# Performance work log

Hardware: AMD Instinct MI355X
Metric: run time of the kernel (lower is better)

The kernel has to match this reference:

```python
import jax, jax.numpy as jnp
import numpy as np
from jax import lax

B, C, H, W = 4096, 10, 30, 30
NCOL = C - 1                      # non-background colors 1..9
_pi, _pj = np.triu_indices(NCOL, 1)  # lexicographic (i<j) pair order, matches the python double loop
PI = jnp.asarray(_pi); PJ = jnp.asarray(_pj)
NPAIR = int(_pi.shape[0])         # 36
W_TRANSFORM, W_EXACT, W_AFFINE, W_ROT, W_REFL, W_GEO, W_EDGE, W_CBAL = 0.2, 7.0, 0.4, 0.3, 0.3, 0.5, 0.3, 0.2
GAMMA = 1.4


def setup_inputs() -> dict:
    key = jax.random.key(0)
    ks = jax.random.split(key, 6)
    pred = jax.random.normal(ks[0], (B, C, H, W), jnp.float32)
    tidx = jax.random.randint(ks[1], (B, H, W), 0, C)
    target = jnp.transpose(jax.nn.one_hot(tidx, C, dtype=jnp.float32), (0, 3, 1, 2))
    iidx = jax.random.randint(ks[2], (B, H, W), 0, C)
    input_grid = jnp.transpose(jax.nn.one_hot(iidx, C, dtype=jnp.float32), (0, 3, 1, 2))
    theta = 0.1 * jax.random.normal(ks[3], (B, 2, 3), jnp.float32)
    rot = jax.random.normal(ks[4], (B, 8), jnp.float32)
    refl = jax.random.normal(ks[5], (B, 4), jnp.float32)
    return {"pred_output": pred, "target_output": target, "input_grid": input_grid,
            "theta": theta, "rotation_logits": rot, "reflection_logits": refl}


def _detect_edges(idx):
    # idx: [B,H,W] int; pixel is an edge if it differs from any h/w neighbor
    dh = idx[:, 1:, :] != idx[:, :-1, :]
    dw = idx[:, :, 1:] != idx[:, :, :-1]
    e = jnp.pad(dh, ((0, 0), (1, 0), (0, 0))) | jnp.pad(dh, ((0, 0), (0, 1), (0, 0)))
    e = e | jnp.pad(dw, ((0, 0), (0, 0), (1, 0))) | jnp.pad(dw, ((0, 0), (0, 0), (0, 1)))
    return e


def _entropy_mean(logits):
    lp = jax.nn.log_softmax(logits, axis=1)
    return (-(jnp.exp(lp) * lp).sum(axis=1)).mean()


def _sobel(idx_f):
    sx = jnp.array([[-1., 0., 1.], [-2., 0., 2.], [-1., 0., 1.]], jnp.float32).reshape(1, 1, 3, 3)
    sy = jnp.array([[-1., -2., -1.], [0., 0., 0.], [1., 2., 1.]], jnp.float32).reshape(1, 1, 3, 3)
    x = idx_f[:, None]  # [B,1,H,W]
    dn = ('NCHW', 'OIHW', 'NCHW')
    ex = lax.conv_general_dilated(x, sx, (1, 1), ((1, 1), (1, 1)), dimension_numbers=dn)
    ey = lax.conv_general_dilated(x, sy, (1, 1), ((1, 1), (1, 1)), dimension_numbers=dn)
    return jnp.sqrt(ex * ex + ey * ey)


def _centers(grid):
    # grid: [H,W] int -> per-color (1..9) center of mass and presence
    cols = jnp.arange(1, C)
    mask = (grid[None] == cols[:, None, None]).astype(jnp.float32)  # [9,H,W]
    cnt = mask.sum((1, 2))
    ys = jnp.arange(H, dtype=jnp.float32)[:, None]
    xs = jnp.arange(W, dtype=jnp.float32)[None, :]
    cy = (mask * ys).sum((1, 2)) / jnp.maximum(cnt, 1.0)
    cx = (mask * xs).sum((1, 2)) / jnp.maximum(cnt, 1.0)
    return cy, cx, cnt > 0


def _compact_dists(cy, cx, present):
    # distances for all 36 color pairs, compacted so valid pairs occupy
    # the leading slots in the same lexicographic order as the torch loops
    d = jnp.sqrt((cy[PI] - cy[PJ]) ** 2 + (cx[PI] - cx[PJ]) ** 2)
    v = present[PI] & present[PJ]
    rank = jnp.cumsum(v.astype(jnp.int32)) - 1
    slot = jnp.where(v, rank, NPAIR)          # dump invalid pairs in scratch slot
    compact = jnp.zeros(NPAIR + 1, jnp.float32).at[slot].set(d)
    return compact[:NPAIR], v.sum()


def _geo_sample(pidx, tidx):
    cyp, cxp, prp = _centers(pidx)
    cyt, cxt, prt = _centers(tidx)
    dp, n_p = _compact_dists(cyp, cxp, prp)
    dt, n_t = _compact_dists(cyt, cxt, prt)
    m = jnp.minimum(n_p, n_t)                 # min_len truncation
    use = jnp.arange(NPAIR) < m
    sq = jnp.where(use, (dp - dt) ** 2, 0.0)
    return jnp.where(m > 0, sq.sum() / jnp.maximum(m, 1).astype(jnp.float32), 0.0)


def _components(pred, target, inp, theta, rot, refl):
    tidx = jnp.argmax(target, axis=1)
    pidx = jnp.argmax(pred, axis=1)
    iidx = jnp.argmax(inp, axis=1)
    # spatial focal CE with edge-weighted pixels
    lp = jax.nn.log_softmax(pred, axis=1)
    ce = -jnp.take_along_axis(lp, tidx[:, None], axis=1)[:, 0]  # [B,H,W]
    pt = jnp.exp(-ce)
    sw = jnp.where(_detect_edges(tidx), 1.5, 1.0)
    spatial_focal = ((1.0 - pt) ** GAMMA * ce * sw).mean()
    # exact match bonus / copy penalty
    exact = jnp.all(pidx == tidx, axis=(1, 2)).astype(jnp.float32)
    exact_count = exact.sum()
    exact_bonus = -exact.mean() * W_EXACT
    copy = jnp.all(pidx == iidx, axis=(1, 2)).astype(jnp.float32)
    transform = copy.mean() * W_TRANSFORM
    # affine regularization on theta
    scale_reg = jnp.sqrt((theta[:, :2, :2] ** 2).sum((1, 2)))
    trans_reg = jnp.sqrt((theta[:, :, 2] ** 2).sum(1))
    affine = (scale_reg.mean() + 0.1 * trans_reg.mean()) * W_AFFINE
    rotation = _entropy_mean(rot) * W_ROT
    reflection = _entropy_mean(refl) * W_REFL
    # geometric color-center consistency (vmapped over batch)
    geo = jax.vmap(_geo_sample)(pidx, tidx).sum() / B * W_GEO
    # sobel edge MSE on argmax indices
    pe = _sobel(pidx.astype(jnp.float32))
    te = _sobel(tidx.astype(jnp.float32))
    edge = jnp.mean((pe - te) ** 2) * W_EDGE
    # color balance
    pc = jax.nn.softmax(pred, axis=1).sum((2, 3))
    tc = target.sum((2, 3))
    pc = pc / (pc.sum(1, keepdims=True) + 1e-8)
    tc = tc / (tc.sum(1, keepdims=True) + 1e-8)
    cbal = jnp.mean((pc - tc) ** 2) * W_CBAL
    total = (spatial_focal + transform + affine + rotation + reflection
             + geo + edge + cbal + exact_bonus)
    return (total, spatial_focal, transform, exact_bonus, exact_count,
            affine, rotation, reflection, geo, edge, cbal)


def reference(pred_output, target_output, input_grid, theta, rotation_logits, reflection_logits):
    return _components(pred_output, target_output, input_grid, theta,
                       rotation_logits, reflection_logits)
```

## Files before the change

kernel.cpp:

```cpp
#include <hip/hip_runtime.h>
#include <stdint.h>

#define B_   4096
#define C_   10
#define H_   30
#define W_   30
#define HW_  900
#define NCOL_ 9
#define NPART 9


__device__ __forceinline__ float entropyN(const float* __restrict__ x, int n) {
    float m = x[0];
    for (int i = 1; i < n; ++i) m = fmaxf(m, x[i]);
    float se = 0.f;
    for (int i = 0; i < n; ++i) se += __expf(x[i] - m);
    float lse = m + __logf(se);
    float ent = 0.f;
    for (int i = 0; i < n; ++i) { float lp = x[i] - lse; ent -= __expf(lp) * lp; }
    return ent;
}


__global__ __launch_bounds__(64) void zero_out_k(float* out, int n) {
    int i = threadIdx.x;
    if (i < n) out[i] = 0.f;
}

__global__ __launch_bounds__(256, 4) void loss_main(
    const float* __restrict__ pred, const float* __restrict__ target,
    const float* __restrict__ inp,  const float* __restrict__ theta,
    const float* __restrict__ rotl, const float* __restrict__ refl,
    float* __restrict__ partials ,
    float* __restrict__ out)
{
    __shared__ uint8_t s_t[33 * 32];
    __shared__ uint8_t s_p[33 * 32];
    __shared__ __align__(16) float s_cef[30 * 36];
    __shared__ unsigned long long s_ctr[2][NCOL_];
    __shared__ float s_wred[4][16];
    __shared__ float s_dp[36], s_dt[36];
    __shared__ float s_cy[2][NCOL_], s_cx[2][NCOL_];
    __shared__ int   s_pr[2][NCOL_];
    __shared__ int   s_tcnt[NCOL_];
    __shared__ float s_small[4];

    const int t = threadIdx.x;
    const int b = blockIdx.x;
    const size_t base = (size_t)b * (C_ * HW_);

    float pc[C_];
#pragma unroll
    for (int c = 0; c < C_; ++c) pc[c] = 0.f;
    float exact_f = 1.f, copy_f = 1.f;

    if (t < 225) {
        const int p0 = 4 * t;
        const float* pp = pred   + base + p0;
        const float* tp = target + base + p0;
        const float* gp = inp    + base + p0;

        float4 pfv[C_];
#pragma unroll
        for (int c = 0; c < C_; ++c)
            pfv[c] = *reinterpret_cast<const float4*>(pp + c * HW_);
        float4 tfv[C_];
#pragma unroll
        for (int c = 0; c < C_; ++c)
            tfv[c] = *reinterpret_cast<const float4*>(tp + c * HW_);

        float vt[4]  = {0.f, 0.f, 0.f, 0.f};
        float tif[4] = {0.f, 0.f, 0.f, 0.f};
        float iif[4] = {0.f, 0.f, 0.f, 0.f};
#pragma unroll
        for (int c = 0; c < C_; ++c) {
            float4 gf = *reinterpret_cast<const float4*>(gp + c * HW_);
            const float4 tf = tfv[c];
            const float4 pf = pfv[c];
            const float fc = (float)c;
            vt[0] = fmaf(tf.x, pf.x, vt[0]); vt[1] = fmaf(tf.y, pf.y, vt[1]);
            vt[2] = fmaf(tf.z, pf.z, vt[2]); vt[3] = fmaf(tf.w, pf.w, vt[3]);
            tif[0] = fmaf(tf.x, fc, tif[0]); tif[1] = fmaf(tf.y, fc, tif[1]);
            tif[2] = fmaf(tf.z, fc, tif[2]); tif[3] = fmaf(tf.w, fc, tif[3]);
            iif[0] = fmaf(gf.x, fc, iif[0]); iif[1] = fmaf(gf.y, fc, iif[1]);
            iif[2] = fmaf(gf.z, fc, iif[2]); iif[3] = fmaf(gf.w, fc, iif[3]);
        }

        int h = p0 / 30;
        int w = p0 - 30 * h;
#pragma unroll
        for (int j = 0; j < 4; ++j) {
            const int ti = (int)tif[j];
            const int ii = (int)iif[j];
            const float* pj = (const float*)&pfv[0];
            float pm = pj[j]; int pi = 0;
            float se = 0.f;
            float ex[C_];
#pragma unroll
            for (int c = 0; c < C_; ++c) {
                const float raw = ((const float*)&pfv[c])[j];
                if (c > 0 && raw > pm) { pm = raw; pi = c; }
                float e = __expf(raw);
                ex[c] = e;
                se += e;
            }
            const float inv = __builtin_amdgcn_rcpf(se);
#pragma unroll
            for (int c = 0; c < C_; ++c) pc[c] = fmaf(ex[c], inv, pc[c]);
            const float ce = __logf(se) - vt[j];

            s_t[(h + 1) * 32 + (w + 1)] = (uint8_t)ti;
            s_p[(h + 1) * 32 + (w + 1)] = (uint8_t)pi;
            s_cef[36 * h + w] = ce;
            if (pi != ti) exact_f = 0.f;
            if (pi != ii) copy_f = 0.f;
            if (++w == 30) { w = 0; ++h; }
        }
    } else if (t < 252) {
        const int z = t - 225;
        for (int k = z; k < 32; k += 27) {
            const int g = k >> 4, r = (k >> 3) & 1, dw = k & 7;
            uint32_t* pb = (uint32_t*)((g ? s_p : s_t) + (r ? 31 * 32 : 0));
            pb[dw] = 0u;
        }
        for (int k = z; k < 120; k += 27) {
            const int g = (k >= 60);
            const int kk = k - 60 * g;
            const int r = 1 + (kk >> 1);
            const int cp = (kk & 1) ? 31 : 0;
            (g ? s_p : s_t)[r * 32 + cp] = 0;
        }
        for (int k = z; k < 2 * NCOL_; k += 27) ((unsigned long long*)s_ctr)[k] = 0ull;
    } else if (t == 252) {
        s_small[0] = entropyN(rotl + (size_t)b * 8, 8);
    } else if (t == 253) {
        s_small[1] = entropyN(refl + (size_t)b * 4, 4);
    } else if (t == 254) {
        const float* th = theta + (size_t)b * 6;
        float sreg = sqrtf(th[0]*th[0] + th[1]*th[1] + th[3]*th[3] + th[4]*th[4]);
        float treg = sqrtf(th[2]*th[2] + th[5]*th[5]);
        s_small[2] = sreg + 0.1f * treg;
    }
    __syncthreads();

    float focal = 0.f, edg = 0.f;
    if (t < 240) {
        const int h = t >> 3, wq = t & 7;
        const int w0 = 4 * wq;
        const int npx = (w0 < 28) ? 4 : 2;

        const uint32_t* tr0 = (const uint32_t*)(s_t + 32 * h);
        const uint32_t* tr1 = (const uint32_t*)(s_t + 32 * (h + 1));
        const uint32_t* tr2 = (const uint32_t*)(s_t + 32 * (h + 2));
        const uint32_t* pr0 = (const uint32_t*)(s_p + 32 * h);
        const uint32_t* pr1 = (const uint32_t*)(s_p + 32 * (h + 1));
        const uint32_t* pr2 = (const uint32_t*)(s_p + 32 * (h + 2));

        uint32_t td[3][2] = {{tr0[wq], tr0[wq + 1]}, {tr1[wq], tr1[wq + 1]}, {tr2[wq], tr2[wq + 1]}};
        uint32_t pd[3][2] = {{pr0[wq], pr0[wq + 1]}, {pr1[wq], pr1[wq + 1]}, {pr2[wq], pr2[wq + 1]}};
        const float4 cef = *reinterpret_cast<const float4*>(s_cef + 36 * h + w0);
        const float cearr[4] = {cef.x, cef.y, cef.z, cef.w};

        int tb[3][6], pb[3][6];
#pragma unroll
        for (int r = 0; r < 3; ++r) {
            const uint32_t d0t = td[r][0], d1t = td[r][1];
            tb[r][0] = d0t & 255; tb[r][1] = (d0t >> 8) & 255; tb[r][2] = (d0t >> 16) & 255;
            tb[r][3] = d0t >> 24; tb[r][4] = d1t & 255; tb[r][5] = (d1t >> 8) & 255;
            const uint32_t d0p = pd[r][0], d1p = pd[r][1];
            pb[r][0] = d0p & 255; pb[r][1] = (d0p >> 8) & 255; pb[r][2] = (d0p >> 16) & 255;
            pb[r][3] = d0p >> 24; pb[r][4] = d1p & 255; pb[r][5] = (d1p >> 8) & 255;
        }
        int s1t[6], s2t[6], s1p[6], s2p[6];
#pragma unroll
        for (int j = 0; j < 6; ++j) {
            s1t[j] = tb[0][j] + 2 * tb[1][j] + tb[2][j];
            s2t[j] = tb[2][j] - tb[0][j];
            s1p[j] = pb[0][j] + 2 * pb[1][j] + pb[2][j];
            s2p[j] = pb[2][j] - pb[0][j];
        }
#pragma unroll
        for (int k = 0; k < 4; ++k) {
            if (k < npx) {
                const int w = w0 + k;
                const int tv = tb[1][k + 1], pv = pb[1][k + 1];
                const bool eg = (h > 0  && tb[0][k + 1] != tv) ||
                                (h < 29 && tb[2][k + 1] != tv) ||
                                (w > 0  && tb[1][k]     != tv) ||
                                (w < 29 && tb[1][k + 2] != tv);
                const float ce = cearr[k];
                const float pt = __expf(-ce);
                const float omt = fmaxf(1.f - pt, 0.f);
                focal += __powf(omt, 1.4f) * ce * (eg ? 1.5f : 1.0f);

                const int ext = s1t[k + 2] - s1t[k];
                const int eyt = s2t[k] + 2 * s2t[k + 1] + s2t[k + 2];
                const int exq = s1p[k + 2] - s1p[k];
                const int eyq = s2p[k] + 2 * s2p[k + 1] + s2p[k + 2];
                const float mt = sqrtf((float)(ext * ext + eyt * eyt));
                const float mp = sqrtf((float)(exq * exq + eyq * eyq));
                const float dd = mp - mt;
                edg += dd * dd;

                const unsigned long long add =
                    (1ull << 42) | ((unsigned long long)(unsigned)h << 21) | (unsigned)w;
                if (tv > 0) atomicAdd(&s_ctr[1][tv - 1], add);
                if (pv > 0) atomicAdd(&s_ctr[0][pv - 1], add);
            }
        }
    }

    float vals[14];
    vals[0] = focal; vals[1] = edg;
#pragma unroll
    for (int c = 0; c < C_; ++c) vals[2 + c] = pc[c];
    vals[12] = exact_f; vals[13] = copy_f;
#pragma unroll
    for (int off = 32; off > 0; off >>= 1) {
#pragma unroll
        for (int k = 0; k < 12; ++k) vals[k] += __shfl_down(vals[k], off);
        vals[12] = fminf(vals[12], __shfl_down(vals[12], off));
        vals[13] = fminf(vals[13], __shfl_down(vals[13], off));
    }
    const int wid = t >> 6, lane = t & 63;
    if (lane == 0) {
#pragma unroll
        for (int k = 0; k < 14; ++k) s_wred[wid][k] = vals[k];
    }
    __syncthreads();

    if (t < 18) {
        const int g = (t >= 9);
        const int k = t - 9 * g;
        const unsigned long long q = s_ctr[g][k];
        const int sx = (int)(q & 0x1FFFFF), sy = (int)((q >> 21) & 0x1FFFFF), cn = (int)(q >> 42);
        const float dn = fmaxf((float)cn, 1.f);
        s_cy[g][k] = (float)sy / dn;
        s_cx[g][k] = (float)sx / dn;
        s_pr[g][k] = (cn > 0);
        if (g) s_tcnt[k] = cn;
    }
    __syncthreads();

    if (t < 64) {
        const int l = t;
        const int i = (l >= 8) + (l >= 15) + (l >= 21) + (l >= 26) +
                      (l >= 30) + (l >= 33) + (l >= 35);
        const int j = l - (i * (17 - i)) / 2 + i + 1;
        bool vp = false, vtp = false;
        float dp = 0.f, dt = 0.f;
        if (l < 36) {
            vp  = s_pr[0][i] && s_pr[0][j];
            vtp = s_pr[1][i] && s_pr[1][j];
            float dyp = s_cy[0][i] - s_cy[0][j], dxp = s_cx[0][i] - s_cx[0][j];
            dp = sqrtf(dyp * dyp + dxp * dxp);
            float dyt = s_cy[1][i] - s_cy[1][j], dxt = s_cx[1][i] - s_cx[1][j];
            dt = sqrtf(dyt * dyt + dxt * dxt);
        }
        const unsigned long long mp_mask = __ballot(vp);
        const unsigned long long mt_mask = __ballot(vtp);
        const unsigned long long below = (1ull << l) - 1ull;
        if (vp)  s_dp[__popcll(mp_mask & below)] = dp;
        if (vtp) s_dt[__popcll(mt_mask & below)] = dt;
        const int np = (int)__popcll(mp_mask);
        const int nt = (int)__popcll(mt_mask);
        const int mm = np < nt ? np : nt;
        float term = 0.f;
        if (l < mm) { float d = s_dp[l] - s_dt[l]; term = d * d; }
#pragma unroll
        for (int off = 32; off > 0; off >>= 1) term += __shfl_down(term, off);

        if (t == 0) {
            const float geo_b = (mm > 0) ? term / (float)mm : 0.f;

            float r[14];
#pragma unroll
            for (int k = 0; k < 14; ++k) r[k] = s_wred[0][k];
            for (int w2 = 1; w2 < 4; ++w2) {
#pragma unroll
                for (int k = 0; k < 12; ++k) r[k] += s_wred[w2][k];
                r[12] = fminf(r[12], s_wred[w2][12]);
                r[13] = fminf(r[13], s_wred[w2][13]);
            }

            float pcs = 0.f;
#pragma unroll
            for (int c = 0; c < C_; ++c) pcs += r[2 + c];
            const float ipcs = 1.f / (pcs + 1e-8f);
            int tsum = 0;
#pragma unroll
            for (int k = 0; k < NCOL_; ++k) tsum += s_tcnt[k];
            float cb = 0.f;
            const float itd = 1.f / (900.f + 1e-8f);
            {
                float d = r[2] * ipcs - (float)(HW_ - tsum) * itd;
                cb += d * d;
            }
#pragma unroll
            for (int c = 1; c < C_; ++c) {
                float d = r[2 + c] * ipcs - (float)s_tcnt[c - 1] * itd;
                cb += d * d;
            }

            float res[NPART];
            res[0] = r[0];
            res[1] = r[12];
            res[2] = r[13];
            res[3] = s_small[2];
            res[4] = s_small[0];
            res[5] = s_small[1];
            res[6] = geo_b;
            res[7] = r[1];
            res[8] = cb;

            if (partials) {
                float* pw = partials + (size_t)b * NPART;
#pragma unroll
                for (int k = 0; k < NPART; ++k) pw[k] = res[k];
            } else {
                atomicAdd(&out[1],  res[0]);
                atomicAdd(&out[2],  res[2]);
                atomicAdd(&out[4],  res[1]);
                atomicAdd(&out[5],  res[3]);
                atomicAdd(&out[6],  res[4]);
                atomicAdd(&out[7],  res[5]);
                atomicAdd(&out[8],  res[6]);
                atomicAdd(&out[9],  res[7]);
                atomicAdd(&out[10], res[8]);
            }
        }
    }
}

__device__ __forceinline__ void write_final(float* out,
    double focal_s, double exact_s, double copy_s, double aff_s,
    double rot_s, double refl_s, double geo_s, double edge_s, double cbal_s)
{
    const double invB = 1.0 / (double)B_;
    float focal      = (float)(focal_s / ((double)B_ * (double)HW_));
    float transform  = (float)(copy_s * invB * 0.2);
    float exact_cnt  = (float)exact_s;
    float exact_bns  = (float)(-(exact_s * invB) * 7.0);
    float affine     = (float)(aff_s * invB * 0.4);
    float rotation   = (float)(rot_s * invB * 0.3);
    float reflection = (float)(refl_s * invB * 0.3);
    float geo        = (float)(geo_s * invB * 0.5);
    float edge       = (float)(edge_s / ((double)B_ * (double)HW_) * 0.3);
    float cbal       = (float)(cbal_s / ((double)B_ * (double)C_) * 0.2);
    out[0] = focal + transform + affine + rotation + reflection + geo + edge + cbal + exact_bns;
    out[1] = focal; out[2] = transform; out[3] = exact_bns; out[4] = exact_cnt;
    out[5] = affine; out[6] = rotation; out[7] = reflection; out[8] = geo;
    out[9] = edge; out[10] = cbal;
}

__global__ __launch_bounds__(256) void reduce_partials(
    const float* __restrict__ partials, float* __restrict__ out)
{
    __shared__ double sh[256][NPART];
    const int t = threadIdx.x;
    double acc[NPART];
#pragma unroll
    for (int k = 0; k < NPART; ++k) acc[k] = 0.0;
    for (int b = t; b < B_; b += 256) {
        const float* pp = partials + (size_t)b * NPART;
#pragma unroll
        for (int k = 0; k < NPART; ++k) acc[k] += (double)pp[k];
    }
#pragma unroll
    for (int k = 0; k < NPART; ++k) sh[t][k] = acc[k];
    __syncthreads();
    for (int s = 128; s > 0; s >>= 1) {
        if (t < s) {
#pragma unroll
            for (int k = 0; k < NPART; ++k) sh[t][k] += sh[t + s][k];
        }
        __syncthreads();
    }
    if (t == 0) {
        write_final(out, sh[0][0], sh[0][1], sh[0][2], sh[0][3],
                    sh[0][4], sh[0][5], sh[0][6], sh[0][7], sh[0][8]);
    }
}

__global__ void finalize_atomic(float* out) {
    if (threadIdx.x == 0) {
        write_final(out, (double)out[1], (double)out[4], (double)out[2], (double)out[5],
                    (double)out[6], (double)out[7], (double)out[8], (double)out[9],
                    (double)out[10]);
    }
}


extern "C" void kernel_launch(void* const* d_in, const int* in_sizes, int n_in,
                              void* d_out, int out_size, void* d_ws, size_t ws_size,
                              hipStream_t stream) {
    const float* pred   = (const float*)d_in[0];
    const float* target = (const float*)d_in[1];
    const float* inp    = (const float*)d_in[2];
    const float* theta  = (const float*)d_in[3];
    const float* rotl   = (const float*)d_in[4];
    const float* refl   = (const float*)d_in[5];
    float* out = (float*)d_out;

    const size_t need = (size_t)B_ * NPART * sizeof(float);
    if (d_ws != nullptr && ws_size >= need) {
        loss_main<<<B_, 256, 0, stream>>>(pred, target, inp, theta, rotl, refl,
                                          (float*)d_ws, out);
        reduce_partials<<<1, 256, 0, stream>>>((const float*)d_ws, out);
    } else {
        zero_out_k<<<1, 64, 0, stream>>>(out, out_size);
        loss_main<<<B_, 256, 0, stream>>>(pred, target, inp, theta, rotl, refl,
                                          nullptr, out);
        finalize_atomic<<<1, 1, 0, stream>>>(out);
    }
}
```

Measured before the change: 94.75 us.

## Use DPP wave reductions, hoist input loads, move focal math to phase one

Replaces the shuffle-based wave reductions with DPP row operations plus a readlane, and replaces the min-reductions of the exact/copy flags with wave ballots (__all). All input-grid loads are hoisted next to the pred and target loads, with a scheduling barrier, to raise memory-level parallelism. The focal base term is computed in the load phase, so the second phase only adds the extra edge weight. Launch bounds occupancy drops from 4 to 3 blocks, which gives more registers per thread but fewer waves in flight. A wait and wave barrier are also added before the shared-memory reads in the geo step.

```diff
diff --git a/kernel.cpp b/kernel.cpp
--- a/kernel.cpp
+++ b/kernel.cpp
@@ -21,13 +21,30 @@
     return ent;
 }
 
+template <int CTRL>
+__device__ __forceinline__ float dpp_add_stage(float x) {
+    int y = __builtin_amdgcn_update_dpp(0, __builtin_bit_cast(int, x),
+                                        CTRL, 0xf, 0xf, true);
+    return x + __builtin_bit_cast(float, y);
+}
+__device__ __forceinline__ float wave_sum64(float x) {
+    x = dpp_add_stage<0x111>(x);
+    x = dpp_add_stage<0x112>(x);
+    x = dpp_add_stage<0x114>(x);
+    x = dpp_add_stage<0x118>(x);
+    x = dpp_add_stage<0x142>(x);
+    x = dpp_add_stage<0x143>(x);
+    return __builtin_bit_cast(float,
+        __builtin_amdgcn_readlane(__builtin_bit_cast(int, x), 63));
+}
+
 
 __global__ __launch_bounds__(64) void zero_out_k(float* out, int n) {
     int i = threadIdx.x;
     if (i < n) out[i] = 0.f;
 }
 
-__global__ __launch_bounds__(256, 4) void loss_main(
+__global__ __launch_bounds__(256, 3) void loss_main(
     const float* __restrict__ pred, const float* __restrict__ target,
     const float* __restrict__ inp,  const float* __restrict__ theta,
     const float* __restrict__ rotl, const float* __restrict__ refl,
@@ -36,7 +53,7 @@
 {
     __shared__ uint8_t s_t[33 * 32];
     __shared__ uint8_t s_p[33 * 32];
-    __shared__ __align__(16) float s_cef[30 * 36];
+    __shared__ __align__(16) float s_fb[30 * 36];
     __shared__ unsigned long long s_ctr[2][NCOL_];
     __shared__ float s_wred[4][16];
     __shared__ float s_dp[36], s_dt[36];
@@ -45,14 +62,17 @@
     __shared__ int   s_tcnt[NCOL_];
     __shared__ float s_small[4];
 
-    const int t = threadIdx.x;
-    const int b = blockIdx.x;
+    const int t    = threadIdx.x;
+    const int wid  = t >> 6;
+    const int lane = t & 63;
+    const int b    = blockIdx.x;
     const size_t base = (size_t)b * (C_ * HW_);
 
     float pc[C_];
 #pragma unroll
     for (int c = 0; c < C_; ++c) pc[c] = 0.f;
-    float exact_f = 1.f, copy_f = 1.f;
+    float focal_base = 0.f, focal_edge = 0.f, edg = 0.f;
+    bool ok_e = true, ok_c = true;
 
     if (t < 225) {
         const int p0 = 4 * t;
@@ -60,23 +80,26 @@
         const float* tp = target + base + p0;
         const float* gp = inp    + base + p0;
 
-        float4 pfv[C_];
+        float4 pfv[C_], tfv[C_], gfv[C_];
 #pragma unroll
         for (int c = 0; c < C_; ++c)
             pfv[c] = *reinterpret_cast<const float4*>(pp + c * HW_);
-        float4 tfv[C_];
 #pragma unroll
         for (int c = 0; c < C_; ++c)
             tfv[c] = *reinterpret_cast<const float4*>(tp + c * HW_);
+#pragma unroll
+        for (int c = 0; c < C_; ++c)
+            gfv[c] = *reinterpret_cast<const float4*>(gp + c * HW_);
+        __builtin_amdgcn_sched_barrier(0);
 
         float vt[4]  = {0.f, 0.f, 0.f, 0.f};
         float tif[4] = {0.f, 0.f, 0.f, 0.f};
         float iif[4] = {0.f, 0.f, 0.f, 0.f};
 #pragma unroll
         for (int c = 0; c < C_; ++c) {
-            float4 gf = *reinterpret_cast<const float4*>(gp + c * HW_);
             const float4 tf = tfv[c];
             const float4 pf = pfv[c];
+            const float4 gf = gfv[c];
             const float fc = (float)c;
             vt[0] = fmaf(tf.x, pf.x, vt[0]); vt[1] = fmaf(tf.y, pf.y, vt[1]);
             vt[2] = fmaf(tf.z, pf.z, vt[2]); vt[3] = fmaf(tf.w, pf.w, vt[3]);
@@ -92,8 +115,7 @@
         for (int j = 0; j < 4; ++j) {
             const int ti = (int)tif[j];
             const int ii = (int)iif[j];
-            const float* pj = (const float*)&pfv[0];
-            float pm = pj[j]; int pi = 0;
+            float pm = ((const float*)&pfv[0])[j]; int pi = 0;
             float se = 0.f;
             float ex[C_];
 #pragma unroll
@@ -108,12 +130,16 @@
 #pragma unroll
             for (int c = 0; c < C_; ++c) pc[c] = fmaf(ex[c], inv, pc[c]);
             const float ce = __logf(se) - vt[j];
+            const float pt = __expf(-ce);
+            const float omt = fmaxf(1.f - pt, 0.f);
+            const float fb = __powf(omt, 1.4f) * ce;
+            focal_base += fb;
 
             s_t[(h + 1) * 32 + (w + 1)] = (uint8_t)ti;
             s_p[(h + 1) * 32 + (w + 1)] = (uint8_t)pi;
-            s_cef[36 * h + w] = ce;
-            if (pi != ti) exact_f = 0.f;
-            if (pi != ii) copy_f = 0.f;
+            s_fb[36 * h + w] = fb;
+            if (pi != ti) ok_e = false;
+            if (pi != ii) ok_c = false;
             if (++w == 30) { w = 0; ++h; }
         }
     } else if (t < 252) {
@@ -143,7 +169,6 @@
     }
     __syncthreads();
 
-    float focal = 0.f, edg = 0.f;
     if (t < 240) {
         const int h = t >> 3, wq = t & 7;
         const int w0 = 4 * wq;
@@ -158,40 +183,37 @@
 
         uint32_t td[3][2] = {{tr0[wq], tr0[wq + 1]}, {tr1[wq], tr1[wq + 1]}, {tr2[wq], tr2[wq + 1]}};
         uint32_t pd[3][2] = {{pr0[wq], pr0[wq + 1]}, {pr1[wq], pr1[wq + 1]}, {pr2[wq], pr2[wq + 1]}};
-        const float4 cef = *reinterpret_cast<const float4*>(s_cef + 36 * h + w0);
-        const float cearr[4] = {cef.x, cef.y, cef.z, cef.w};
-
-        int tb[3][6], pb[3][6];
+        const float4 fbf = *reinterpret_cast<const float4*>(s_fb + 36 * h + w0);
+        const float fbarr[4] = {fbf.x, fbf.y, fbf.z, fbf.w};
+
+        int tb2[3][6], pb2[3][6];
 #pragma unroll
         for (int r = 0; r < 3; ++r) {
             const uint32_t d0t = td[r][0], d1t = td[r][1];
-            tb[r][0] = d0t & 255; tb[r][1] = (d0t >> 8) & 255; tb[r][2] = (d0t >> 16) & 255;
-            tb[r][3] = d0t >> 24; tb[r][4] = d1t & 255; tb[r][5] = (d1t >> 8) & 255;
+            tb2[r][0] = d0t & 255; tb2[r][1] = (d0t >> 8) & 255; tb2[r][2] = (d0t >> 16) & 255;
+            tb2[r][3] = d0t >> 24; tb2[r][4] = d1t & 255; tb2[r][5] = (d1t >> 8) & 255;
             const uint32_t d0p = pd[r][0], d1p = pd[r][1];
-            pb[r][0] = d0p & 255; pb[r][1] = (d0p >> 8) & 255; pb[r][2] = (d0p >> 16) & 255;
-            pb[r][3] = d0p >> 24; pb[r][4] = d1p & 255; pb[r][5] = (d1p >> 8) & 255;
+            pb2[r][0] = d0p & 255; pb2[r][1] = (d0p >> 8) & 255; pb2[r][2] = (d0p >> 16) & 255;
+            pb2[r][3] = d0p >> 24; pb2[r][4] = d1p & 255; pb2[r][5] = (d1p >> 8) & 255;
         }
         int s1t[6], s2t[6], s1p[6], s2p[6];
 #pragma unroll
         for (int j = 0; j < 6; ++j) {
-            s1t[j] = tb[0][j] + 2 * tb[1][j] + tb[2][j];
-            s2t[j] = tb[2][j] - tb[0][j];
-            s1p[j] = pb[0][j] + 2 * pb[1][j] + pb[2][j];
-            s2p[j] = pb[2][j] - pb[0][j];
+            s1t[j] = tb2[0][j] + 2 * tb2[1][j] + tb2[2][j];
+            s2t[j] = tb2[2][j] - tb2[0][j];
+            s1p[j] = pb2[0][j] + 2 * pb2[1][j] + pb2[2][j];
+            s2p[j] = pb2[2][j] - pb2[0][j];
         }
 #pragma unroll
         for (int k = 0; k < 4; ++k) {
             if (k < npx) {
                 const int w = w0 + k;
-                const int tv = tb[1][k + 1], pv = pb[1][k + 1];
-                const bool eg = (h > 0  && tb[0][k + 1] != tv) ||
-                                (h < 29 && tb[2][k + 1] != tv) ||
-                                (w > 0  && tb[1][k]     != tv) ||
-                                (w < 29 && tb[1][k + 2] != tv);
-                const float ce = cearr[k];
-                const float pt = __expf(-ce);
-                const float omt = fmaxf(1.f - pt, 0.f);
-                focal += __powf(omt, 1.4f) * ce * (eg ? 1.5f : 1.0f);
+                const int tv = tb2[1][k + 1], pv2 = pb2[1][k + 1];
+                const bool eg = (h > 0  && tb2[0][k + 1] != tv) ||
+                                (h < 29 && tb2[2][k + 1] != tv) ||
+                                (w > 0  && tb2[1][k]     != tv) ||
+                                (w < 29 && tb2[1][k + 2] != tv);
+                if (eg) focal_edge += fbarr[k];
 
                 const int ext = s1t[k + 2] - s1t[k];
                 const int eyt = s2t[k] + 2 * s2t[k + 1] + s2t[k + 2];
@@ -204,28 +226,26 @@
 
                 const unsigned long long add =
                     (1ull << 42) | ((unsigned long long)(unsigned)h << 21) | (unsigned)w;
-                if (tv > 0) atomicAdd(&s_ctr[1][tv - 1], add);
-                if (pv > 0) atomicAdd(&s_ctr[0][pv - 1], add);
-            }
-        }
-    }
-
-    float vals[14];
-    vals[0] = focal; vals[1] = edg;
+                if (tv  > 0) atomicAdd(&s_ctr[1][tv  - 1], add);
+                if (pv2 > 0) atomicAdd(&s_ctr[0][pv2 - 1], add);
+            }
+        }
+    }
+
+    float vals[12];
+    vals[0] = focal_base + 0.5f * focal_edge;
+    vals[1] = edg;
 #pragma unroll
     for (int c = 0; c < C_; ++c) vals[2 + c] = pc[c];
-    vals[12] = exact_f; vals[13] = copy_f;
-#pragma unroll
-    for (int off = 32; off > 0; off >>= 1) {
-#pragma unroll
-        for (int k = 0; k < 12; ++k) vals[k] += __shfl_down(vals[k], off);
-        vals[12] = fminf(vals[12], __shfl_down(vals[12], off));
-        vals[13] = fminf(vals[13], __shfl_down(vals[13], off));
-    }
-    const int wid = t >> 6, lane = t & 63;
+#pragma unroll
+    for (int k = 0; k < 12; ++k) vals[k] = wave_sum64(vals[k]);
+    const int all_e = __all(ok_e);
+    const int all_c = __all(ok_c);
     if (lane == 0) {
 #pragma unroll
-        for (int k = 0; k < 14; ++k) s_wred[wid][k] = vals[k];
+        for (int k = 0; k < 12; ++k) s_wred[wid][k] = vals[k];
+        s_wred[wid][12] = (float)all_e;
+        s_wred[wid][13] = (float)all_c;
     }
     __syncthreads();
 
@@ -265,6 +285,8 @@
         const int np = (int)__popcll(mp_mask);
         const int nt = (int)__popcll(mt_mask);
         const int mm = np < nt ? np : nt;
+        asm volatile("s_waitcnt lgkmcnt(0)" ::: "memory");
+        __builtin_amdgcn_wave_barrier();
         float term = 0.f;
         if (l < mm) { float d = s_dp[l] - s_dt[l]; term = d * d; }
 #pragma unroll
```

Result: faster. 92.05 us (-2.8%).
